# Performance work log

Measured on AMD Instinct MI355X. Metric: run time of the kernel, lower is better.

The kernel has to match this reference:

```python
import jax, jax.numpy as jnp
import numpy as np

B, L, DIM, H, DQK, DV = 4, 512, 1024, 8, 64, 64
ANGLE_BASE = 1.0 / 1024.0
EPS = 1e-5


def _xavier(key, out_d, in_d, gain):
    bound = gain * np.sqrt(6.0 / (in_d + out_d))
    return jax.random.uniform(key, (out_d, in_d), jnp.float32, -bound, bound)


def setup_inputs():
    key = jax.random.key(0)
    ks = jax.random.split(key, 9)
    # p_angle buffer: angle_base ** linspace(0,1,H*DQK) reshaped to [H, DQK]
    p_angle = (ANGLE_BASE ** jnp.linspace(0.0, 1.0, H * DQK)).reshape(H, DQK)
    return {
        "x": jax.random.normal(ks[0], (B, L, DIM), jnp.float32),
        "hidden": 0.1 * jax.random.normal(ks[1], (B, H, DQK, DV, 2), jnp.float32),
        "w_qk": _xavier(ks[2], H * DQK * 4, DIM, 0.01), "b_qk": jnp.zeros((H * DQK * 4,), jnp.float32),
        "w_v": _xavier(ks[3], H * DV * 2, DIM, 0.01), "b_v": jnp.zeros((H * DV * 2,), jnp.float32),
        "w_g": _xavier(ks[4], H * DV * 2, DIM, 0.01), "b_g": jnp.zeros((H * DV * 2,), jnp.float32),
        "w_a": _xavier(ks[5], H, DIM, 1e-4), "b_a": jnp.zeros((H,), jnp.float32),
        "w_y": _xavier(ks[6], DIM, H * DV * 2, 0.01), "b_y": jnp.zeros((DIM,), jnp.float32),
        "gn_w": jnp.ones((H,), jnp.float32), "gn_b": jnp.zeros((H,), jnp.float32),
        "p_angle": p_angle,
    }


def _sioconv(x, hidden, w_qk, b_qk, w_v, b_v, w_g, b_g, w_a, b_a, w_y, b_y, gn_w, gn_b, p_angle):
    b, l = x.shape[0], x.shape[1]
    hid = hidden[..., 0] + 1j * hidden[..., 1]                       # [B,H,I,V] complex
    v_r = (x @ w_v.T + b_v).reshape(b, l, H, DV, 2)
    v = v_r[..., 0] + 1j * v_r[..., 1]                                # [B,L,H,V]
    qk_r = (x @ w_qk.T + b_qk).reshape(b, l, H, DQK, 2, 2)
    qk = qk_r[..., 0] + 1j * qk_r[..., 1]                             # [B,L,H,I,2]
    q, k = qk[..., 0], qk[..., 1]
    a_angle = x @ w_a.T + b_a                                         # [B,L,H]
    ln_a = (1j * a_angle - 1.0) * p_angle[:, 0]                       # [B,L,H] complex
    t = jnp.arange(l, dtype=jnp.float32)
    ppq = jnp.exp(1j * (t[:, None, None] * p_angle[None]))            # [L,H,I] = exp(+i*angle*l)
    qp = q * ppq[None]
    kp = k * jnp.conj(ppq)[None]                                      # exp(-i*angle*l)
    # Decay matrix. The FFT conv with ones computes a causal prefix sum, so
    # c[b,h,l,m] = exp(sum_{j=m+1..l} ln_a[b,j,h]) for m<=l, else 0.
    S = jnp.cumsum(ln_a, axis=1)                                      # [B,L,H]
    Sh = jnp.transpose(S, (0, 2, 1))                                  # [B,H,L]
    mask = jnp.tril(jnp.ones((l, l), bool))
    diff = jnp.where(mask, Sh[:, :, :, None] - Sh[:, :, None, :], 0.0)
    c = jnp.where(mask, jnp.exp(diff), 0.0)                           # [B,H,L,L]
    qck = jnp.einsum('blhi,bmhi->bhlm', qp, kp) * c
    h_inner = jnp.einsum('bhlm,bmhv->blhv', qck, v)
    d = jnp.exp(S)                                                    # [B,L,H] cumulative decay
    p1 = jnp.exp(1j * p_angle)                                        # [H,I]
    h_cross = jnp.einsum('blhi,bhiv->blhv', qp * d[..., None], hid * p1[None, :, :, None])
    h = h_inner + h_cross                                             # [B,L,H,V]
    pp_inv = jnp.exp(1j * ((l - 1.0 - t)[:, None, None] * p_angle[None]))  # [L,H,I]
    hid_next = jnp.einsum('blhi,bhl,lhi,blhv->bhiv', k, c[:, :, -1, :], pp_inv, v)
    hid_next = hid_next + jnp.exp(S[:, -1, :])[:, :, None, None] * hid * jnp.exp(1j * p_angle * l)[None, :, :, None]
    # GroupNorm(num_head, num_head) on real view [B*L, H, V, 2]: normalize over (V,2) per head.
    hr = jnp.stack([h.real, h.imag], axis=-1)                         # [B,L,H,V,2]
    mu = hr.mean(axis=(3, 4), keepdims=True)
    var = hr.var(axis=(3, 4), keepdims=True)
    hn = (hr - mu) / jnp.sqrt(var + EPS)
    hn = hn * gn_w[None, None, :, None, None] + gn_b[None, None, :, None, None]
    h_flat = hn.reshape(b, l, H * DV * 2)
    g = x @ w_g.T + b_g
    y = (h_flat * (g * jax.nn.sigmoid(g))) @ w_y.T + b_y
    return y, hid_next


def reference(x, hidden, w_qk, b_qk, w_v, b_v, w_g, b_g, w_a, b_a, w_y, b_y, gn_w, gn_b, p_angle):
    return _sioconv(x, hidden, w_qk, b_qk, w_v, b_v, w_g, b_g, w_a, b_a, w_y, b_y, gn_w, gn_b, p_angle)
```

## Files before the change

kernel.cpp:

```cpp
#include <hip/hip_runtime.h>
#include <cstdint>
#include <cstddef>

#define B_   4
#define L_   512
#define DIM_ 1024
#define H_   8
#define DQK_ 64
#define DV_  64
#define M_   (B_ * L_)
#define EPS_ 1e-5f

typedef __attribute__((ext_vector_type(8))) short short8;
typedef __attribute__((ext_vector_type(4))) float f32x4;

__device__ __forceinline__ unsigned short f2bf(float f) {
    uint32_t u = __float_as_uint(f);
    u += 0x7FFFu + ((u >> 16) & 1u);
    return (unsigned short)(u >> 16);
}

__device__ __forceinline__ f32x4 mm16(short8 a, short8 b, f32x4 c) {
    return __builtin_amdgcn_mfma_f32_16x16x32_bf16(a, b, c, 0, 0, 0);
}

__device__ __forceinline__ int swoff(int r, int kb) {
    return r * 128 + (kb ^ ((r & 7) << 4));
}
__device__ __forceinline__ short8 frag(const unsigned short* p, int strip, int ks, int lane) {
    const int fr = lane & 15, fq = lane >> 4;
    const int r = strip * 16 + fr;
    return *(const short8*)((const char*)p + swoff(r, ks * 64 + fq * 16));
}

__global__ __launch_bounds__(256) void cast_plus_a(
    const float* __restrict__ x, const float* __restrict__ wqk,
    const float* __restrict__ wv, const float* __restrict__ wg,
    const float* __restrict__ wy,
    unsigned short* __restrict__ xb, unsigned short* __restrict__ wqkb,
    unsigned short* __restrict__ wvb, unsigned short* __restrict__ wgb,
    unsigned short* __restrict__ wyb,
    const float* __restrict__ wa, const float* __restrict__ ba,
    float* __restrict__ a_out)
{
    const int blk = blockIdx.x;
    if (blk < 7168) {
        const float* src; unsigned short* dst; int base;
        if      (blk < 2048) { src = x;   dst = xb;   base = blk; }
        else if (blk < 4096) { src = wqk; dst = wqkb; base = blk - 2048; }
        else if (blk < 5120) { src = wv;  dst = wvb;  base = blk - 4096; }
        else if (blk < 6144) { src = wg;  dst = wgb;  base = blk - 5120; }
        else                 { src = wy;  dst = wyb;  base = blk - 6144; }
        const int i = base * 256 + threadIdx.x;
        const float4 v = ((const float4*)src)[i];
        ushort4 o;
        o.x = f2bf(v.x); o.y = f2bf(v.y); o.z = f2bf(v.z); o.w = f2bf(v.w);
        ((ushort4*)dst)[i] = o;
    } else {
        const int w    = threadIdx.x >> 6;
        const int lane = threadIdx.x & 63;
        const int oidx = (blk - 7168) * 4 + w;
        const int r = oidx >> 3, h = oidx & 7;
        const float* xr = x + (size_t)r * DIM_;
        const float* wr = wa + (size_t)h * DIM_;
        float p = 0.f;
        for (int k = lane; k < DIM_; k += 64)
            p = fmaf(xr[k], wr[k], p);
#pragma unroll
        for (int off = 32; off; off >>= 1)
            p += __shfl_down(p, off);
        if (lane == 0) a_out[oidx] = p + ba[h];
    }
}

__device__ __forceinline__ void gload16(const void* g, void* l) {
    __builtin_amdgcn_global_load_lds(
        (const __attribute__((address_space(1))) unsigned int*)g,
        (__attribute__((address_space(3))) unsigned int*)l, 16, 0, 0);
}

__global__ __launch_bounds__(256) void gemm_mfma(
    const unsigned short* __restrict__ A, const unsigned short* __restrict__ W,
    const float* __restrict__ bias0, const float* __restrict__ bias1,
    const float* __restrict__ bias2,
    float* __restrict__ C0, float* __restrict__ C1, float* __restrict__ C2,
    int n1, int n2, int ld0, int ld1, int ld2, int M, int N, int K)
{
    __shared__ unsigned short sA[128 * 32];
    __shared__ unsigned short sB[128 * 32];

    const int t    = threadIdx.x;
    const int lane = t & 63;
    const int wv   = t >> 6;
    const int bm   = blockIdx.y * 128;
    const int bn   = blockIdx.x * 128;
    const int wr   = wv >> 1, wc = wv & 1;
    const int fr   = lane & 15;
    const int fq   = lane >> 4;
    const int srow = lane >> 2;
    const int ske  = (lane & 3) * 8;

    f32x4 acc[4][4] = {};

    for (int k0 = 0; k0 < K; k0 += 32) {
#pragma unroll
        for (int q = 0; q < 2; ++q) {
            const int c2 = wv * 2 + q;
            gload16(A + (size_t)(bm + c2 * 16 + srow) * K + k0 + ske,
                    (char*)sA + c2 * 1024);
            gload16(W + (size_t)(bn + c2 * 16 + srow) * K + k0 + ske,
                    (char*)sB + c2 * 1024);
        }
        __syncthreads();

        short8 af[4], bf[4];
#pragma unroll
        for (int mi = 0; mi < 4; ++mi)
            af[mi] = *(const short8*)&sA[(wr * 64 + mi * 16 + fr) * 32 + fq * 8];
#pragma unroll
        for (int ni = 0; ni < 4; ++ni)
            bf[ni] = *(const short8*)&sB[(wc * 64 + ni * 16 + fr) * 32 + fq * 8];
#pragma unroll
        for (int mi = 0; mi < 4; ++mi)
#pragma unroll
            for (int ni = 0; ni < 4; ++ni)
                acc[mi][ni] = mm16(af[mi], bf[ni], acc[mi][ni]);
        __syncthreads();
    }

    float* Cb; const float* bb; int coff, ldc;
    if      (bn < n1) { Cb = C0; bb = bias0; coff = 0;  ldc = ld0; }
    else if (bn < n2) { Cb = C1; bb = bias1; coff = n1; ldc = ld1; }
    else              { Cb = C2; bb = bias2; coff = n2; ldc = ld2; }

#pragma unroll
    for (int mi = 0; mi < 4; ++mi)
#pragma unroll
        for (int ni = 0; ni < 4; ++ni) {
            const int col = bn + wc * 64 + ni * 16 + fr - coff;
            const float bv = bb[col];
#pragma unroll
            for (int r = 0; r < 4; ++r) {
                const int row = bm + wr * 64 + mi * 16 + fq * 4 + r;
                Cb[(size_t)row * ldc + col] = acc[mi][ni][r] + bv;
            }
        }
}

__global__ __launch_bounds__(256) void chunkA_mfma(
    const float* __restrict__ qk_raw, const float* __restrict__ vbuf,
    const float* __restrict__ a_ang, const float* __restrict__ p_angle,
    float* __restrict__ h_pre, float* __restrict__ Zloc,
    float* __restrict__ Gbuf, float* __restrict__ Wbuf)
{
    const int blk = blockIdx.x;
    const int c  = blk & 7;
    const int bh = blk >> 3;
    const int b = bh >> 3, h = bh & 7;
    const int t = threadIdx.x;
    const int l0 = c * 64;

    __shared__ unsigned short pQr[4096], pQi[4096];
    __shared__ unsigned short pKr[4096], pKi[4096];
    __shared__ unsigned short pKtr[4096], pKti[4096];
    __shared__ unsigned short pVtr[4096], pVti[4096];
    __shared__ float sW[64][4];
    __shared__ float sTh[64];

    if (t < 64) {
        sTh[t] = p_angle[h * DQK_ + t];
        const float th0 = p_angle[h * DQK_];
        const float a = a_ang[((size_t)(b * L_) + l0 + t) * H_ + h];
        float sa, ca; __sincosf(a * th0, &sa, &ca);
        const float em = expf(-th0), ep = expf(th0);
        float lr = em * ca, li = em * sa;
        float ir = ep * ca, ii = -ep * sa;
#pragma unroll
        for (int off = 1; off < 64; off <<= 1) {
            const float plr = __shfl_up(lr, off);
            const float pli = __shfl_up(li, off);
            const float pir = __shfl_up(ir, off);
            const float pii = __shfl_up(ii, off);
            if (t >= off) {
                float nr = lr * plr - li * pli;
                float ni = lr * pli + li * plr;
                lr = nr; li = ni;
                nr = ir * pir - ii * pii;
                ni = ir * pii + ii * pir;
                ir = nr; ii = ni;
            }
        }
        sW[t][0] = lr; sW[t][1] = li; sW[t][2] = ir; sW[t][3] = ii;
        Wbuf[((size_t)bh * L_ + l0 + t) * 2 + 0] = lr;
        Wbuf[((size_t)bh * L_ + l0 + t) * 2 + 1] = li;
        if (t == 63) {
            Gbuf[(bh * 8 + c) * 2 + 0] = lr;
            Gbuf[(bh * 8 + c) * 2 + 1] = li;
        }
    }
    __syncthreads();

    const int row = t >> 2, cs = t & 3;
    {
        const float wr = sW[row][0], wi = sW[row][1];
        const float xr = sW[row][2], xi = sW[row][3];
        const float lf = (float)(l0 + row);
        unsigned short qr16[16], qi16[16], kr16[16], ki16[16];
        const float4* qg = (const float4*)(qk_raw +
            (((size_t)(b * L_ + l0 + row) * H_ + h) * 64 + cs * 16) * 4);
#pragma unroll
        for (int j = 0; j < 16; ++j) {
            const float4 q = qg[j];
            float sn, cn; __sincosf(sTh[cs * 16 + j] * lf, &sn, &cn);
            const float fqr = cn * wr - sn * wi, fqi = cn * wi + sn * wr;
            const float fkr = cn * xr + sn * xi, fki = cn * xi - sn * xr;
            qr16[j] = f2bf(q.x * fqr - q.y * fqi);
            qi16[j] = f2bf(q.x * fqi + q.y * fqr);
            const float kr = q.z * fkr - q.w * fki;
            const float ki = q.z * fki + q.w * fkr;
            kr16[j] = f2bf(kr); ki16[j] = f2bf(ki);
            const int i = cs * 16 + j;
            const int ob = swoff(i, 2 * row);
            *(unsigned short*)((char*)pKtr + ob) = kr16[j];
            *(unsigned short*)((char*)pKti + ob) = ki16[j];
        }
        const int kb0 = 32 * cs;
        short8 s0, s1;
#pragma unroll
        for (int j = 0; j < 8; ++j) { s0[j] = (short)qr16[j]; s1[j] = (short)qr16[8 + j]; }
        *(short8*)((char*)pQr + swoff(row, kb0))      = s0;
        *(short8*)((char*)pQr + swoff(row, kb0 + 16)) = s1;
#pragma unroll
        for (int j = 0; j < 8; ++j) { s0[j] = (short)qi16[j]; s1[j] = (short)qi16[8 + j]; }
        *(short8*)((char*)pQi + swoff(row, kb0))      = s0;
        *(short8*)((char*)pQi + swoff(row, kb0 + 16)) = s1;
#pragma unroll
        for (int j = 0; j < 8; ++j) { s0[j] = (short)kr16[j]; s1[j] = (short)kr16[8 + j]; }
        *(short8*)((char*)pKr + swoff(row, kb0))      = s0;
        *(short8*)((char*)pKr + swoff(row, kb0 + 16)) = s1;
#pragma unroll
        for (int j = 0; j < 8; ++j) { s0[j] = (short)ki16[j]; s1[j] = (short)ki16[8 + j]; }
        *(short8*)((char*)pKi + swoff(row, kb0))      = s0;
        *(short8*)((char*)pKi + swoff(row, kb0 + 16)) = s1;

        const float2* vg = (const float2*)(vbuf +
            (((size_t)(b * L_ + l0 + row) * H_ + h) * 64 + cs * 16) * 2);
#pragma unroll
        for (int j = 0; j < 16; ++j) {
            const float2 vv = vg[j];
            const int v = cs * 16 + j;
            const int ob = swoff(v, 2 * row);
            *(unsigned short*)((char*)pVtr + ob) = f2bf(vv.x);
            *(unsigned short*)((char*)pVti + ob) = f2bf(vv.y);
        }
    }
    __syncthreads();

    const int w = t >> 6, lane = t & 63;
    const int fr = lane & 15, fq = lane >> 4;
    short8 aQr0 = frag(pQr, w, 0, lane), aQr1 = frag(pQr, w, 1, lane);
    short8 aQi0 = frag(pQi, w, 0, lane), aQi1 = frag(pQi, w, 1, lane);
    f32x4 Pr[4], Pi[4];
#pragma unroll
    for (int tm = 0; tm < 4; ++tm) {
        short8 bKr0 = frag(pKr, tm, 0, lane), bKr1 = frag(pKr, tm, 1, lane);
        short8 bKi0 = frag(pKi, tm, 0, lane), bKi1 = frag(pKi, tm, 1, lane);
        f32x4 tmp = {};
        tmp = mm16(aQi0, bKi0, tmp); tmp = mm16(aQi1, bKi1, tmp);
        tmp = -tmp;
        tmp = mm16(aQr0, bKr0, tmp); tmp = mm16(aQr1, bKr1, tmp);
        Pr[tm] = tmp;
        f32x4 t2 = {};
        t2 = mm16(aQr0, bKi0, t2); t2 = mm16(aQr1, bKi1, t2);
        t2 = mm16(aQi0, bKr0, t2); t2 = mm16(aQi1, bKr1, t2);
        Pi[tm] = t2;
    }
#pragma unroll
    for (int tm = 0; tm < 4; ++tm) {
        const int m = tm * 16 + fr;
#pragma unroll
        for (int r = 0; r < 4; ++r) {
            const int l = w * 16 + fq * 4 + r;
            const int ob = swoff(l, 2 * m);
            const float prv = (m <= l) ? Pr[tm][r] : 0.f;
            const float piv = (m <= l) ? Pi[tm][r] : 0.f;
            *(unsigned short*)((char*)pQr + ob) = f2bf(prv);
            *(unsigned short*)((char*)pQi + ob) = f2bf(piv);
        }
    }

    short8 aPr0 = frag(pQr, w, 0, lane), aPr1 = frag(pQr, w, 1, lane);
    short8 aPi0 = frag(pQi, w, 0, lane), aPi1 = frag(pQi, w, 1, lane);
    short8 aKt_r0 = frag(pKtr, w, 0, lane), aKt_r1 = frag(pKtr, w, 1, lane);
    short8 aKt_i0 = frag(pKti, w, 0, lane), aKt_i1 = frag(pKti, w, 1, lane);
    const float Gr = sW[63][0], Gi = sW[63][1];
#pragma unroll
    for (int tv = 0; tv < 4; ++tv) {
        short8 bVr0 = frag(pVtr, tv, 0, lane), bVr1 = frag(pVtr, tv, 1, lane);
        short8 bVi0 = frag(pVti, tv, 0, lane), bVi1 = frag(pVti, tv, 1, lane);
        f32x4 hr = {};
        hr = mm16(aPi0, bVi0, hr); hr = mm16(aPi1, bVi1, hr);
        hr = -hr;
        hr = mm16(aPr0, bVr0, hr); hr = mm16(aPr1, bVr1, hr);
        f32x4 hi = {};
        hi = mm16(aPr0, bVi0, hi); hi = mm16(aPr1, bVi1, hi);
        hi = mm16(aPi0, bVr0, hi); hi = mm16(aPi1, bVr1, hi);
        f32x4 zr = {};
        zr = mm16(aKt_i0, bVi0, zr); zr = mm16(aKt_i1, bVi1, zr);
        zr = -zr;
        zr = mm16(aKt_r0, bVr0, zr); zr = mm16(aKt_r1, bVr1, zr);
        f32x4 zi = {};
        zi = mm16(aKt_r0, bVi0, zi); zi = mm16(aKt_r1, bVi1, zi);
        zi = mm16(aKt_i0, bVr0, zi); zi = mm16(aKt_i1, bVr1, zi);
#pragma unroll
        for (int r = 0; r < 4; ++r) {
            const int lrow = w * 16 + fq * 4 + r;
            const int v = tv * 16 + fr;
            *(float2*)(h_pre + (((size_t)(b * L_ + l0 + lrow) * H_ + h) * 64 + v) * 2)
                = make_float2(hr[r], hi[r]);
            float* zp = Zloc + (((size_t)(bh * 8 + c) * 4096) + lrow * 64 + v) * 2;
            zp[0] = Gr * zr[r] - Gi * zi[r];
            zp[1] = Gr * zi[r] + Gi * zr[r];
        }
    }
}

__global__ __launch_bounds__(512) void scanB(
    float* __restrict__ Zbuf, const float* __restrict__ Gbuf,
    const float* __restrict__ hidden, const float* __restrict__ p_angle,
    float* __restrict__ hid_out, int real_only)
{
    const int bid = blockIdx.x;
    const int bh = bid >> 3, part = bid & 7;
    const int h = bh & 7;
    const int e = part * 512 + threadIdx.x;
    const int i = e >> 6;
    const float th = p_angle[h * 64 + i];
    float s, c; __sincosf(th, &s, &c);
    const float2 h0 = *(const float2*)(hidden + ((size_t)bh * 4096 + e) * 2);
    float zr = h0.x * c - h0.y * s;
    float zi = h0.x * s + h0.y * c;
#pragma unroll
    for (int ch = 0; ch < 8; ++ch) {
        float* zp = Zbuf + ((size_t)(bh * 8 + ch) * 4096 + e) * 2;
        const float zlr = zp[0], zli = zp[1];
        zp[0] = zr; zp[1] = zi;
        const float gr = Gbuf[(bh * 8 + ch) * 2], gi = Gbuf[(bh * 8 + ch) * 2 + 1];
        const float nr = gr * zr - gi * zi + zlr;
        const float ni = gr * zi + gi * zr + zli;
        zr = nr; zi = ni;
    }
    float s2, c2; __sincosf(th * (float)(L_ - 1), &s2, &c2);
    const float outr = zr * c2 - zi * s2;
    const float outi = zr * s2 + zi * c2;
    if (real_only) {
        hid_out[(size_t)bh * 4096 + e] = outr;
    } else {
        hid_out[((size_t)bh * 4096 + e) * 2 + 0] = outr;
        hid_out[((size_t)bh * 4096 + e) * 2 + 1] = outi;
    }
}

__global__ __launch_bounds__(256) void chunkC_gn(
    const float* __restrict__ qk_raw, const float* __restrict__ Wbuf,
    const float* __restrict__ Zin, const float* __restrict__ p_angle,
    const float* __restrict__ h_intra, const float* __restrict__ gbuf,
    const float* __restrict__ gn_w, const float* __restrict__ gn_b,
    unsigned short* __restrict__ act)
{
    const int blk = blockIdx.x;
    const int c = blk & 7, bh = blk >> 3;
    const int b = bh >> 3, h = bh & 7;
    const int t = threadIdx.x;
    const int l0 = c * 64;

    __shared__ unsigned short pQr[4096], pQi[4096];
    __shared__ unsigned short pZtr[4096], pZti[4096];
    __shared__ float sTh[64];

    if (t < 64) sTh[t] = p_angle[h * 64 + t];
    __syncthreads();

    const int row = t >> 2, cs = t & 3;
    {
        const float wr = Wbuf[((size_t)bh * L_ + l0 + row) * 2];
        const float wi = Wbuf[((size_t)bh * L_ + l0 + row) * 2 + 1];
        const float lf = (float)(l0 + row);
        unsigned short qr16[16], qi16[16];
        const float4* qg = (const float4*)(qk_raw +
            (((size_t)(b * L_ + l0 + row) * H_ + h) * 64 + cs * 16) * 4);
#pragma unroll
        for (int j = 0; j < 16; ++j) {
            const float4 q = qg[j];
            float sn, cn; __sincosf(sTh[cs * 16 + j] * lf, &sn, &cn);
            const float fqr = cn * wr - sn * wi, fqi = cn * wi + sn * wr;
            qr16[j] = f2bf(q.x * fqr - q.y * fqi);
            qi16[j] = f2bf(q.x * fqi + q.y * fqr);
        }
        const int kb0 = 32 * cs;
        short8 s0, s1;
#pragma unroll
        for (int j = 0; j < 8; ++j) { s0[j] = (short)qr16[j]; s1[j] = (short)qr16[8 + j]; }
        *(short8*)((char*)pQr + swoff(row, kb0))      = s0;
        *(short8*)((char*)pQr + swoff(row, kb0 + 16)) = s1;
#pragma unroll
        for (int j = 0; j < 8; ++j) { s0[j] = (short)qi16[j]; s1[j] = (short)qi16[8 + j]; }
        *(short8*)((char*)pQi + swoff(row, kb0))      = s0;
        *(short8*)((char*)pQi + swoff(row, kb0 + 16)) = s1;

        const float2* zg = (const float2*)(Zin +
            ((size_t)(bh * 8 + c) * 4096 + row * 64 + cs * 16) * 2);
#pragma unroll
        for (int j = 0; j < 16; ++j) {
            const float2 z = zg[j];
            const int v = cs * 16 + j;
            const int ob = swoff(v, 2 * row);
            *(unsigned short*)((char*)pZtr + ob) = f2bf(z.x);
            *(unsigned short*)((char*)pZti + ob) = f2bf(z.y);
        }
    }
    __syncthreads();

    const int w = t >> 6, lane = t & 63;
    const int fr = lane & 15, fq = lane >> 4;
    short8 aQr0 = frag(pQr, w, 0, lane), aQr1 = frag(pQr, w, 1, lane);
    short8 aQi0 = frag(pQi, w, 0, lane), aQi1 = frag(pQi, w, 1, lane);

    float hreg[4][4][2];
#pragma unroll
    for (int tv = 0; tv < 4; ++tv) {
        short8 bZr0 = frag(pZtr, tv, 0, lane), bZr1 = frag(pZtr, tv, 1, lane);
        short8 bZi0 = frag(pZti, tv, 0, lane), bZi1 = frag(pZti, tv, 1, lane);
        f32x4 hr = {};
        hr = mm16(aQi0, bZi0, hr); hr = mm16(aQi1, bZi1, hr);
        hr = -hr;
        hr = mm16(aQr0, bZr0, hr); hr = mm16(aQr1, bZr1, hr);
        f32x4 hi = {};
        hi = mm16(aQr0, bZi0, hi); hi = mm16(aQr1, bZi1, hi);
        hi = mm16(aQi0, bZr0, hi); hi = mm16(aQi1, bZr1, hi);
#pragma unroll
        for (int r = 0; r < 4; ++r) {
            const int l = w * 16 + fq * 4 + r;
            const int v = tv * 16 + fr;
            const float2 hin = *(const float2*)(h_intra +
                (((size_t)(b * L_ + l0 + l) * H_ + h) * 64 + v) * 2);
            hreg[tv][r][0] = hin.x + hr[r];
            hreg[tv][r][1] = hin.y + hi[r];
        }
    }

    const float gw = gn_w[h], gbn = gn_b[h];
    float mean4[4], scl4[4];
#pragma unroll
    for (int r = 0; r < 4; ++r) {
        float s = 0.f, q = 0.f;
#pragma unroll
        for (int tv = 0; tv < 4; ++tv) {
            s += hreg[tv][r][0] + hreg[tv][r][1];
            q += hreg[tv][r][0] * hreg[tv][r][0] + hreg[tv][r][1] * hreg[tv][r][1];
        }
#pragma unroll
        for (int off = 1; off < 16; off <<= 1) {
            s += __shfl_xor(s, off);
            q += __shfl_xor(q, off);
        }
        const float m = s * (1.f / 128.f);
        const float var = q * (1.f / 128.f) - m * m;
        mean4[r] = m;
        scl4[r] = rsqrtf(var + EPS_) * gw;
    }

#pragma unroll
    for (int tv = 0; tv < 4; ++tv) {
#pragma unroll
        for (int r = 0; r < 4; ++r) {
            const int l = w * 16 + fq * 4 + r;
            const int v = tv * 16 + fr;
            const size_t base = (size_t)(b * L_ + l0 + l) * 1024 + h * 128 + v * 2;
            const float2 gv = *(const float2*)(gbuf + base);
            const float hn0 = (hreg[tv][r][0] - mean4[r]) * scl4[r] + gbn;
            const float hn1 = (hreg[tv][r][1] - mean4[r]) * scl4[r] + gbn;
            const float a0 = hn0 * gv.x / (1.f + expf(-gv.x));
            const float a1 = hn1 * gv.y / (1.f + expf(-gv.y));
            ushort2 o; o.x = f2bf(a0); o.y = f2bf(a1);
            *(ushort2*)(act + base) = o;
        }
    }
}

extern "C" void kernel_launch(void* const* d_in, const int* in_sizes, int n_in,
                              void* d_out, int out_size, void* d_ws, size_t ws_size,
                              hipStream_t stream)
{
    (void)in_sizes; (void)n_in; (void)ws_size;
    const float* x       = (const float*)d_in[0];
    const float* hidden  = (const float*)d_in[1];
    const float* w_qk    = (const float*)d_in[2];
    const float* b_qk    = (const float*)d_in[3];
    const float* w_v     = (const float*)d_in[4];
    const float* b_v     = (const float*)d_in[5];
    const float* w_g     = (const float*)d_in[6];
    const float* b_g     = (const float*)d_in[7];
    const float* w_a     = (const float*)d_in[8];
    const float* b_a     = (const float*)d_in[9];
    const float* w_y     = (const float*)d_in[10];
    const float* b_y     = (const float*)d_in[11];
    const float* gn_w    = (const float*)d_in[12];
    const float* gn_b    = (const float*)d_in[13];
    const float* p_angle = (const float*)d_in[14];

    float* y_out   = (float*)d_out;
    float* hid_out = (float*)d_out + (size_t)M_ * DIM_;
    const int hid_elems = out_size - M_ * DIM_;
    const int real_only = (hid_elems == B_ * H_ * DQK_ * DV_) ? 1 : 0;

    float* ws = (float*)d_ws;
    float* buf_qk  = ws;
    float* buf_v   = buf_qk  + (size_t)M_ * H_ * DQK_ * 4;
    float* buf_g   = buf_v   + (size_t)M_ * H_ * DV_ * 2;
    float* buf_a   = buf_g   + (size_t)M_ * H_ * DV_ * 2;
    float* buf_W   = buf_a   + (size_t)M_ * H_;
    float* buf_G   = buf_W   + 32 * L_ * 2;
    float* buf_Z   = buf_G   + 512;
    float* buf_h   = buf_Z   + (size_t)32 * 8 * 4096 * 2;
    float* buf_wyb = buf_h   + (size_t)M_ * H_ * DV_ * 2 + 262144;

    unsigned short* wqkb = (unsigned short*)buf_Z;
    unsigned short* wvb  = (unsigned short*)(buf_Z + 1048576);
    unsigned short* wgb  = (unsigned short*)(buf_Z + 1572864);
    unsigned short* xb   = (unsigned short*)buf_h;
    unsigned short* wyb  = (unsigned short*)buf_wyb;
    unsigned short* actb = (unsigned short*)buf_v;

    cast_plus_a<<<11264, 256, 0, stream>>>(x, w_qk, w_v, w_g, w_y,
                                           xb, wqkb, wvb, wgb, wyb,
                                           w_a, b_a, buf_a);

    gemm_mfma<<<dim3(32, 16), 256, 0, stream>>>(
        xb, wqkb, b_qk, b_v, b_g, buf_qk, buf_v, buf_g,
        2048, 3072, 2048, 1024, 1024, M_, 4096, DIM_);

    chunkA_mfma<<<B_*H_*8, 256, 0, stream>>>(
        buf_qk, buf_v, buf_a, p_angle, buf_h, buf_Z, buf_G, buf_W);
    scanB<<<B_*H_*8, 512, 0, stream>>>(
        buf_Z, buf_G, hidden, p_angle, hid_out, real_only);
    chunkC_gn<<<B_*H_*8, 256, 0, stream>>>(
        buf_qk, buf_W, buf_Z, p_angle, buf_h, buf_g, gn_w, gn_b, actb);

    gemm_mfma<<<dim3(8, 16), 256, 0, stream>>>(
        actb, wyb, b_y, b_y, b_y, y_out, y_out, y_out,
        1024, 1024, 1024, 1024, 1024, M_, 1024, DIM_);
}
```

Baseline: 106.8 us.

## Fuse a-projection into main GEMM, emit bf16 qk/v, narrow output GEMM tiles

Result: faster. 95.62 us (-10.5%).

```diff
diff --git a/kernel.cpp b/kernel.cpp
--- a/kernel.cpp
+++ b/kernel.cpp
@@ -19,6 +19,9 @@
     u += 0x7FFFu + ((u >> 16) & 1u);
     return (unsigned short)(u >> 16);
 }
+__device__ __forceinline__ float bf2f(unsigned short u) {
+    return __uint_as_float((uint32_t)u << 16);
+}
 
 __device__ __forceinline__ f32x4 mm16(short8 a, short8 b, f32x4 c) {
     return __builtin_amdgcn_mfma_f32_16x16x32_bf16(a, b, c, 0, 0, 0);
@@ -33,44 +36,32 @@
     return *(const short8*)((const char*)p + swoff(r, ks * 64 + fq * 16));
 }
 
-__global__ __launch_bounds__(256) void cast_plus_a(
+__global__ __launch_bounds__(256) void cast_all(
     const float* __restrict__ x, const float* __restrict__ wqk,
     const float* __restrict__ wv, const float* __restrict__ wg,
-    const float* __restrict__ wy,
-    unsigned short* __restrict__ xb, unsigned short* __restrict__ wqkb,
-    unsigned short* __restrict__ wvb, unsigned short* __restrict__ wgb,
-    unsigned short* __restrict__ wyb,
-    const float* __restrict__ wa, const float* __restrict__ ba,
-    float* __restrict__ a_out)
+    const float* __restrict__ wy, const float* __restrict__ wa,
+    const float* __restrict__ ba,
+    unsigned short* __restrict__ xb, unsigned short* __restrict__ wall,
+    unsigned short* __restrict__ wyb, float* __restrict__ babias)
 {
     const int blk = blockIdx.x;
-    if (blk < 7168) {
-        const float* src; unsigned short* dst; int base;
-        if      (blk < 2048) { src = x;   dst = xb;   base = blk; }
-        else if (blk < 4096) { src = wqk; dst = wqkb; base = blk - 2048; }
-        else if (blk < 5120) { src = wv;  dst = wvb;  base = blk - 4096; }
-        else if (blk < 6144) { src = wg;  dst = wgb;  base = blk - 5120; }
-        else                 { src = wy;  dst = wyb;  base = blk - 6144; }
-        const int i = base * 256 + threadIdx.x;
-        const float4 v = ((const float4*)src)[i];
-        ushort4 o;
-        o.x = f2bf(v.x); o.y = f2bf(v.y); o.z = f2bf(v.z); o.w = f2bf(v.w);
-        ((ushort4*)dst)[i] = o;
-    } else {
-        const int w    = threadIdx.x >> 6;
-        const int lane = threadIdx.x & 63;
-        const int oidx = (blk - 7168) * 4 + w;
-        const int r = oidx >> 3, h = oidx & 7;
-        const float* xr = x + (size_t)r * DIM_;
-        const float* wr = wa + (size_t)h * DIM_;
-        float p = 0.f;
-        for (int k = lane; k < DIM_; k += 64)
-            p = fmaf(xr[k], wr[k], p);
-#pragma unroll
-        for (int off = 32; off; off >>= 1)
-            p += __shfl_down(p, off);
-        if (lane == 0) a_out[oidx] = p + ba[h];
-    }
+    if (blk == 7176) {
+        if (threadIdx.x < 128)
+            babias[threadIdx.x] = (threadIdx.x < 8) ? ba[threadIdx.x] : 0.f;
+        return;
+    }
+    const float* src; unsigned short* dst; int base;
+    if      (blk < 2048) { src = x;   dst = xb;                  base = blk; }
+    else if (blk < 4096) { src = wqk; dst = wall;                base = blk - 2048; }
+    else if (blk < 5120) { src = wv;  dst = wall + 2048 * 1024;  base = blk - 4096; }
+    else if (blk < 6144) { src = wg;  dst = wall + 3072 * 1024;  base = blk - 5120; }
+    else if (blk < 7168) { src = wy;  dst = wyb;                 base = blk - 6144; }
+    else                 { src = wa;  dst = wall + 4096 * 1024;  base = blk - 7168; }
+    const int i = base * 256 + threadIdx.x;
+    const float4 v = ((const float4*)src)[i];
+    ushort4 o;
+    o.x = f2bf(v.x); o.y = f2bf(v.y); o.z = f2bf(v.z); o.w = f2bf(v.w);
+    ((ushort4*)dst)[i] = o;
 }
 
 __device__ __forceinline__ void gload16(const void* g, void* l) {
@@ -79,12 +70,16 @@
         (__attribute__((address_space(3))) unsigned int*)l, 16, 0, 0);
 }
 
-__global__ __launch_bounds__(256) void gemm_mfma(
+__global__ __launch_bounds__(256) void gemm_proj(
     const unsigned short* __restrict__ A, const unsigned short* __restrict__ W,
     const float* __restrict__ bias0, const float* __restrict__ bias1,
-    const float* __restrict__ bias2,
-    float* __restrict__ C0, float* __restrict__ C1, float* __restrict__ C2,
-    int n1, int n2, int ld0, int ld1, int ld2, int M, int N, int K)
+    const float* __restrict__ bias2, const float* __restrict__ bias3,
+    void* __restrict__ C0, void* __restrict__ C1,
+    void* __restrict__ C2, void* __restrict__ C3,
+    int n1, int n2, int n3,
+    int ld0, int ld1, int ld2, int ld3,
+    int bf0, int bf1, int bf2, int bf3,
+    int M, int N, int K)
 {
     __shared__ unsigned short sA[128 * 32];
     __shared__ unsigned short sB[128 * 32];
@@ -128,10 +123,11 @@
         __syncthreads();
     }
 
-    float* Cb; const float* bb; int coff, ldc;
-    if      (bn < n1) { Cb = C0; bb = bias0; coff = 0;  ldc = ld0; }
-    else if (bn < n2) { Cb = C1; bb = bias1; coff = n1; ldc = ld1; }
-    else              { Cb = C2; bb = bias2; coff = n2; ldc = ld2; }
+    void* Cb; const float* bb; int coff, ldc, isbf;
+    if      (bn < n1) { Cb = C0; bb = bias0; coff = 0;  ldc = ld0; isbf = bf0; }
+    else if (bn < n2) { Cb = C1; bb = bias1; coff = n1; ldc = ld1; isbf = bf1; }
+    else if (bn < n3) { Cb = C2; bb = bias2; coff = n2; ldc = ld2; isbf = bf2; }
+    else              { Cb = C3; bb = bias3; coff = n3; ldc = ld3; isbf = bf3; }
 
 #pragma unroll
     for (int mi = 0; mi < 4; ++mi)
@@ -142,14 +138,78 @@
 #pragma unroll
             for (int r = 0; r < 4; ++r) {
                 const int row = bm + wr * 64 + mi * 16 + fq * 4 + r;
-                Cb[(size_t)row * ldc + col] = acc[mi][ni][r] + bv;
+                const float val = acc[mi][ni][r] + bv;
+                if (isbf)
+                    ((unsigned short*)Cb)[(size_t)row * ldc + col] = f2bf(val);
+                else
+                    ((float*)Cb)[(size_t)row * ldc + col] = val;
             }
         }
 }
 
+__global__ __launch_bounds__(256) void gemm_y64(
+    const unsigned short* __restrict__ A, const unsigned short* __restrict__ W,
+    const float* __restrict__ bias, float* __restrict__ C,
+    int M, int N, int K)
+{
+    __shared__ unsigned short sA[128 * 32];
+    __shared__ unsigned short sB[64 * 32];
+
+    const int t    = threadIdx.x;
+    const int lane = t & 63;
+    const int wv   = t >> 6;
+    const int bm   = blockIdx.y * 128;
+    const int bn   = blockIdx.x * 64;
+    const int fr   = lane & 15;
+    const int fq   = lane >> 4;
+    const int srow = lane >> 2;
+    const int ske  = (lane & 3) * 8;
+
+    f32x4 acc[2][4] = {};
+
+    for (int k0 = 0; k0 < K; k0 += 32) {
+#pragma unroll
+        for (int q = 0; q < 2; ++q) {
+            const int c2 = wv * 2 + q;
+            gload16(A + (size_t)(bm + c2 * 16 + srow) * K + k0 + ske,
+                    (char*)sA + c2 * 1024);
+        }
+        gload16(W + (size_t)(bn + wv * 16 + srow) * K + k0 + ske,
+                (char*)sB + wv * 1024);
+        __syncthreads();
+
+        short8 af[2], bf[4];
+#pragma unroll
+        for (int mi = 0; mi < 2; ++mi)
+            af[mi] = *(const short8*)&sA[(wv * 32 + mi * 16 + fr) * 32 + fq * 8];
+#pragma unroll
+        for (int ni = 0; ni < 4; ++ni)
+            bf[ni] = *(const short8*)&sB[(ni * 16 + fr) * 32 + fq * 8];
+#pragma unroll
+        for (int mi = 0; mi < 2; ++mi)
+#pragma unroll
+            for (int ni = 0; ni < 4; ++ni)
+                acc[mi][ni] = mm16(af[mi], bf[ni], acc[mi][ni]);
+        __syncthreads();
+    }
+
+#pragma unroll
+    for (int mi = 0; mi < 2; ++mi)
+#pragma unroll
+        for (int ni = 0; ni < 4; ++ni) {
+            const int col = bn + ni * 16 + fr;
+            const float bv = bias[col];
+#pragma unroll
+            for (int r = 0; r < 4; ++r) {
+                const int row = bm + wv * 32 + mi * 16 + fq * 4 + r;
+                C[(size_t)row * N + col] = acc[mi][ni][r] + bv;
+            }
+        }
+}
+
 __global__ __launch_bounds__(256) void chunkA_mfma(
-    const float* __restrict__ qk_raw, const float* __restrict__ vbuf,
-    const float* __restrict__ a_ang, const float* __restrict__ p_angle,
+    const unsigned short* __restrict__ qk_bf, const unsigned short* __restrict__ v_bf,
+    const float* __restrict__ a_pad, const float* __restrict__ p_angle,
     float* __restrict__ h_pre, float* __restrict__ Zloc,
     float* __restrict__ Gbuf, float* __restrict__ Wbuf)
 {
@@ -170,7 +230,7 @@
     if (t < 64) {
         sTh[t] = p_angle[h * DQK_ + t];
         const float th0 = p_angle[h * DQK_];
-        const float a = a_ang[((size_t)(b * L_) + l0 + t) * H_ + h];
+        const float a = a_pad[((size_t)(b * L_) + l0 + t) * 128 + h];
         float sa, ca; __sincosf(a * th0, &sa, &ca);
         const float em = expf(-th0), ep = expf(th0);
         float lr = em * ca, li = em * sa;
@@ -206,18 +266,20 @@
         const float xr = sW[row][2], xi = sW[row][3];
         const float lf = (float)(l0 + row);
         unsigned short qr16[16], qi16[16], kr16[16], ki16[16];
-        const float4* qg = (const float4*)(qk_raw +
-            (((size_t)(b * L_ + l0 + row) * H_ + h) * 64 + cs * 16) * 4);
+        const unsigned short* qg = qk_bf +
+            (size_t)(b * L_ + l0 + row) * 2048 + h * 256 + cs * 64;
 #pragma unroll
         for (int j = 0; j < 16; ++j) {
-            const float4 q = qg[j];
+            const ushort4 qu = *(const ushort4*)(qg + j * 4);
+            const float qre = bf2f(qu.x), qim = bf2f(qu.y);
+            const float kre = bf2f(qu.z), kim = bf2f(qu.w);
             float sn, cn; __sincosf(sTh[cs * 16 + j] * lf, &sn, &cn);
             const float fqr = cn * wr - sn * wi, fqi = cn * wi + sn * wr;
             const float fkr = cn * xr + sn * xi, fki = cn * xi - sn * xr;
-            qr16[j] = f2bf(q.x * fqr - q.y * fqi);
-            qi16[j] = f2bf(q.x * fqi + q.y * fqr);
-            const float kr = q.z * fkr - q.w * fki;
-            const float ki = q.z * fki + q.w * fkr;
+            qr16[j] = f2bf(qre * fqr - qim * fqi);
+            qi16[j] = f2bf(qre * fqi + qim * fqr);
+            const float kr = kre * fkr - kim * fki;
+            const float ki = kre * fki + kim * fkr;
             kr16[j] = f2bf(kr); ki16[j] = f2bf(ki);
             const int i = cs * 16 + j;
             const int ob = swoff(i, 2 * row);
@@ -243,15 +305,15 @@
         *(short8*)((char*)pKi + swoff(row, kb0))      = s0;
         *(short8*)((char*)pKi + swoff(row, kb0 + 16)) = s1;
 
-        const float2* vg = (const float2*)(vbuf +
-            (((size_t)(b * L_ + l0 + row) * H_ + h) * 64 + cs * 16) * 2);
+        const unsigned short* vg = v_bf +
+            (size_t)(b * L_ + l0 + row) * 1024 + h * 128 + cs * 32;
 #pragma unroll
         for (int j = 0; j < 16; ++j) {
-            const float2 vv = vg[j];
+            const ushort2 vv = *(const ushort2*)(vg + j * 2);
             const int v = cs * 16 + j;
             const int ob = swoff(v, 2 * row);
-            *(unsigned short*)((char*)pVtr + ob) = f2bf(vv.x);
-            *(unsigned short*)((char*)pVti + ob) = f2bf(vv.y);
+            *(unsigned short*)((char*)pVtr + ob) = vv.x;
+            *(unsigned short*)((char*)pVti + ob) = vv.y;
         }
     }
     __syncthreads();
@@ -362,7 +424,7 @@
 }
 
 __global__ __launch_bounds__(256) void chunkC_gn(
-    const float* __restrict__ qk_raw, const float* __restrict__ Wbuf,
+    const unsigned short* __restrict__ qk_bf, const float* __restrict__ Wbuf,
     const float* __restrict__ Zin, const float* __restrict__ p_angle,
     const float* __restrict__ h_intra, const float* __restrict__ gbuf,
     const float* __restrict__ gn_w, const float* __restrict__ gn_b,
@@ -387,15 +449,16 @@
         const float wi = Wbuf[((size_t)bh * L_ + l0 + row) * 2 + 1];
         const float lf = (float)(l0 + row);
         unsigned short qr16[16], qi16[16];
-        const float4* qg = (const float4*)(qk_raw +
-            (((size_t)(b * L_ + l0 + row) * H_ + h) * 64 + cs * 16) * 4);
+        const unsigned short* qg = qk_bf +
+            (size_t)(b * L_ + l0 + row) * 2048 + h * 256 + cs * 64;
 #pragma unroll
         for (int j = 0; j < 16; ++j) {
-            const float4 q = qg[j];
+            const ushort4 qu = *(const ushort4*)(qg + j * 4);
+            const float qre = bf2f(qu.x), qim = bf2f(qu.y);
             float sn, cn; __sincosf(sTh[cs * 16 + j] * lf, &sn, &cn);
             const float fqr = cn * wr - sn * wi, fqi = cn * wi + sn * wr;
-            qr16[j] = f2bf(q.x * fqr - q.y * fqi);
-            qi16[j] = f2bf(q.x * fqi + q.y * fqr);
+            qr16[j] = f2bf(qre * fqr - qim * fqi);
+            qi16[j] = f2bf(qre * fqi + qim * fqr);
         }
         const int kb0 = 32 * cs;
         short8 s0, s1;
@@ -514,40 +577,38 @@
     const int hid_elems = out_size - M_ * DIM_;
     const int real_only = (hid_elems == B_ * H_ * DQK_ * DV_) ? 1 : 0;
 
-    float* ws = (float*)d_ws;
-    float* buf_qk  = ws;
-    float* buf_v   = buf_qk  + (size_t)M_ * H_ * DQK_ * 4;
-    float* buf_g   = buf_v   + (size_t)M_ * H_ * DV_ * 2;
-    float* buf_a   = buf_g   + (size_t)M_ * H_ * DV_ * 2;
-    float* buf_W   = buf_a   + (size_t)M_ * H_;
-    float* buf_G   = buf_W   + 32 * L_ * 2;
-    float* buf_Z   = buf_G   + 512;
-    float* buf_h   = buf_Z   + (size_t)32 * 8 * 4096 * 2;
-    float* buf_wyb = buf_h   + (size_t)M_ * H_ * DV_ * 2 + 262144;
-
-    unsigned short* wqkb = (unsigned short*)buf_Z;
-    unsigned short* wvb  = (unsigned short*)(buf_Z + 1048576);
-    unsigned short* wgb  = (unsigned short*)(buf_Z + 1572864);
-    unsigned short* xb   = (unsigned short*)buf_h;
-    unsigned short* wyb  = (unsigned short*)buf_wyb;
-    unsigned short* actb = (unsigned short*)buf_v;
-
-    cast_plus_a<<<11264, 256, 0, stream>>>(x, w_qk, w_v, w_g, w_y,
-                                           xb, wqkb, wvb, wgb, wyb,
-                                           w_a, b_a, buf_a);
-
-    gemm_mfma<<<dim3(32, 16), 256, 0, stream>>>(
-        xb, wqkb, b_qk, b_v, b_g, buf_qk, buf_v, buf_g,
-        2048, 3072, 2048, 1024, 1024, M_, 4096, DIM_);
+    unsigned short* xb     = (unsigned short*)d_ws;
+    unsigned short* wall   = xb   + (size_t)2048 * 1024;
+    unsigned short* wyb    = wall + (size_t)4224 * 1024;
+    unsigned short* bqk    = wyb  + (size_t)1024 * 1024;
+    unsigned short* bv     = bqk  + (size_t)2048 * 2048;
+    unsigned short* actb   = bv   + (size_t)2048 * 1024;
+    float* bg     = (float*)(actb + (size_t)2048 * 1024);
+    float* ba_pad = bg     + (size_t)2048 * 1024;
+    float* babias = ba_pad + (size_t)2048 * 128;
+    float* bufW   = babias + 128;
+    float* bufG   = bufW   + 32 * 512 * 2;
+    float* bufZ   = bufG   + 512;
+    float* bufh   = bufZ   + (size_t)32 * 8 * 4096 * 2;
+
+    cast_all<<<7177, 256, 0, stream>>>(x, w_qk, w_v, w_g, w_y, w_a, b_a,
+                                       xb, wall, wyb, babias);
+
+    gemm_proj<<<dim3(33, 16), 256, 0, stream>>>(
+        xb, wall, b_qk, b_v, b_g, babias,
+        bqk, bv, bg, ba_pad,
+        2048, 3072, 4096,
+        2048, 1024, 1024, 128,
+        1, 1, 0, 0,
+        M_, 4224, DIM_);
 
     chunkA_mfma<<<B_*H_*8, 256, 0, stream>>>(
-        buf_qk, buf_v, buf_a, p_angle, buf_h, buf_Z, buf_G, buf_W);
+        bqk, bv, ba_pad, p_angle, bufh, bufZ, bufG, bufW);
     scanB<<<B_*H_*8, 512, 0, stream>>>(
-        buf_Z, buf_G, hidden, p_angle, hid_out, real_only);
+        bufZ, bufG, hidden, p_angle, hid_out, real_only);
     chunkC_gn<<<B_*H_*8, 256, 0, stream>>>(
-        buf_qk, buf_W, buf_Z, p_angle, buf_h, buf_g, gn_w, gn_b, actb);
-
-    gemm_mfma<<<dim3(8, 16), 256, 0, stream>>>(
-        actb, wyb, b_y, b_y, b_y, y_out, y_out, y_out,
-        1024, 1024, 1024, 1024, 1024, M_, 1024, DIM_);
-}
+        bqk, bufW, bufZ, p_angle, bufh, bg, gn_w, gn_b, actb);
+
+    gemm_y64<<<dim3(16, 16), 256, 0, stream>>>(
+        actb, wyb, b_y, y_out, M_, DIM_, DIM_);
+}
```
